# Kernel tuning notes

Hardware: AMD Instinct MI355X
Metric: run time of the kernel (lower is better)

## Reference

```python
import jax, jax.numpy as jnp
import numpy as np

C = 256
NH = 8
G = 32  # groupnorm groups (min(32, C))
EPS = 1e-6


def setup_inputs() -> dict:
    key = jax.random.key(0)
    ks = jax.random.split(key, 7)
    B, D, H, W = 2, 16, 16, 16
    x = jax.random.normal(ks[0], (B, C, D, H, W), dtype=jnp.float32)
    gn_gamma = jnp.ones((C,), jnp.float32)
    gn_beta = jnp.zeros((C,), jnp.float32)
    s = 1.0 / np.sqrt(C)
    qkv_w = jax.random.normal(ks[1], (3 * C, C), jnp.float32) * s  # 1x1x1 conv weight
    qkv_b = jnp.zeros((3 * C,), jnp.float32)
    proj_w = jax.random.normal(ks[2], (C, C), jnp.float32) * s
    proj_b = jnp.zeros((C,), jnp.float32)
    return {"x": x, "gn_gamma": gn_gamma, "gn_beta": gn_beta,
            "qkv_w": qkv_w, "qkv_b": qkv_b, "proj_w": proj_w, "proj_b": proj_b}


def _group_norm(x, gamma, beta):
    # x: [B, C, S]
    B, Cc, S = x.shape
    xg = x.reshape(B, G, (Cc // G) * S)
    mu = xg.mean(axis=-1, keepdims=True)
    var = xg.var(axis=-1, keepdims=True)
    xg = (xg - mu) * jax.lax.rsqrt(var + EPS)
    x = xg.reshape(B, Cc, S)
    return x * gamma[None, :, None] + beta[None, :, None]


def reference(x, gn_gamma, gn_beta, qkv_w, qkv_b, proj_w, proj_b):
    B, Cc, D, H, W = x.shape
    S = D * H * W
    hd = Cc // NH
    xf = x.reshape(B, Cc, S)
    h = _group_norm(xf, gn_gamma, gn_beta)
    # 1x1x1 conv == channel matmul: [B, 3C, S]
    qkv = jnp.einsum('oc,bcs->bos', qkv_w, h) + qkv_b[None, :, None]
    # torch path: reshape(B,3C,S).permute(0,2,1).chunk -> q=channels[0:C]
    q, k, v = qkv[:, :Cc], qkv[:, Cc:2 * Cc], qkv[:, 2 * Cc:]
    # [B, C, S] -> [B, NH, S, hd]
    def to_heads(t):
        return t.reshape(B, NH, hd, S).transpose(0, 1, 3, 2)
    q, k, v = to_heads(q), to_heads(k), to_heads(v)
    scale = hd ** (-0.5)
    attn = jax.nn.softmax(jnp.einsum('bnqd,bnkd->bnqk', q, k) * scale, axis=-1)
    o = jnp.einsum('bnqk,bnkd->bnqd', attn, v)  # [B, NH, S, hd]
    o = o.transpose(0, 1, 3, 2).reshape(B, Cc, S)  # back to [B, C, S]
    o = jnp.einsum('oc,bcs->bos', proj_w, o) + proj_b[None, :, None]
    return x + o.reshape(B, Cc, D, H, W)
```

## Files before the change

### kernel.cpp

```cpp
#include <hip/hip_runtime.h>
#include <cstddef>

#define S_LEN 4096
#define C_DIM 256
#define NHEADS 8
#define HDIM 32

typedef __attribute__((ext_vector_type(8))) _Float16 half8;
typedef __attribute__((ext_vector_type(4))) _Float16 half4;
typedef __attribute__((ext_vector_type(2))) _Float16 h2t;
typedef __attribute__((ext_vector_type(2))) __fp16 fp16x2;
typedef __attribute__((ext_vector_type(4))) float floatx4;

#define SC2F ((float)(0.17677669529663687 * 1.4426950408889634))

__global__ __launch_bounds__(256) void prep_stats(
    const float* __restrict__ qkv_w, const float* __restrict__ proj_w,
    const float* __restrict__ qkv_b, const float* __restrict__ x,
    _Float16* __restrict__ wq, _Float16* __restrict__ wp,
    float* __restrict__ qbias, float* __restrict__ gstat)
{
  const int blk = blockIdx.x;
  const int tid = threadIdx.x;
  if (blk < 64) {
    __shared__ float red[2][4];
    const int g = blk & 31, b = blk >> 5;
    const float* xb = x + ((size_t)b * C_DIM + g * 8) * S_LEN;
    const float4* x4 = (const float4*)xb;
    float sum = 0.f, sumsq = 0.f;
    for (int i = tid; i < 8192; i += 256) {
      float4 v = x4[i];
      sum += v.x + v.y + v.z + v.w;
      sumsq += v.x * v.x + v.y * v.y + v.z * v.z + v.w * v.w;
    }
    for (int off = 1; off < 64; off <<= 1) {
      sum += __shfl_xor(sum, off, 64);
      sumsq += __shfl_xor(sumsq, off, 64);
    }
    const int wv = tid >> 6, lane = tid & 63;
    if (lane == 0) { red[0][wv] = sum; red[1][wv] = sumsq; }
    __syncthreads();
    if (tid == 0) {
      float s = red[0][0] + red[0][1] + red[0][2] + red[0][3];
      float sq = red[1][0] + red[1][1] + red[1][2] + red[1][3];
      float mean = s * (1.f / 32768.f);
      float var = sq * (1.f / 32768.f) - mean * mean;
      gstat[((size_t)b * 32 + g) * 2 + 0] = mean;
      gstat[((size_t)b * 32 + g) * 2 + 1] = rsqrtf(var + 1e-6f);
    }
  } else {
    int idx = (blk - 64) * 256 + tid;
    if (idx < 768 * 256) {
      float v = qkv_w[idx];
      if (idx < 256 * 256) v *= SC2F;
      wq[idx] = (_Float16)v;
    } else if (idx < 768 * 256 + 256 * 256) {
      int i = idx - 768 * 256;
      wp[i] = (_Float16)proj_w[i];
    } else if (idx < 768 * 256 + 256 * 256 + 768) {
      int i = idx - (768 * 256 + 256 * 256);
      float bv = qkv_b[i];
      if (i < 256) bv *= SC2F;
      qbias[i] = bv;
    }
  }
}

__global__ __launch_bounds__(256) void qkv_gn_gemm(
    const _Float16* __restrict__ W, const float* __restrict__ bias,
    const float* __restrict__ x, const float* __restrict__ gamma,
    const float* __restrict__ beta, const float* __restrict__ gstat,
    _Float16* __restrict__ qo, _Float16* __restrict__ ko_,
    _Float16* __restrict__ vo)
{
  __shared__ __align__(16) _Float16 Ld[64 * 264];
  const int tid = threadIdx.x;
  const int b = blockIdx.z;
  const int s0 = blockIdx.y * 64;

  {
    const int c0 = (tid & 127) * 2, c1 = c0 + 1;
    const int sh = tid >> 7;
    const int g = c0 >> 3;
    const float mean = gstat[((size_t)b * 32 + g) * 2 + 0];
    const float rstd = gstat[((size_t)b * 32 + g) * 2 + 1];
    const float ga0 = gamma[c0] * rstd, be0 = beta[c0] - mean * ga0;
    const float ga1 = gamma[c1] * rstd, be1 = beta[c1] - mean * ga1;
    const float4* xa = (const float4*)(x + ((size_t)b * C_DIM + c0) * S_LEN + s0 + sh * 32);
    const float4* xc = (const float4*)(x + ((size_t)b * C_DIM + c1) * S_LEN + s0 + sh * 32);
    #pragma unroll
    for (int j = 0; j < 8; ++j) {
      float4 a = xa[j], c = xc[j];
      int sl = sh * 32 + j * 4;
      *(h2t*)&Ld[(sl + 0) * 264 + c0] = (h2t){ (_Float16)(a.x * ga0 + be0), (_Float16)(c.x * ga1 + be1) };
      *(h2t*)&Ld[(sl + 1) * 264 + c0] = (h2t){ (_Float16)(a.y * ga0 + be0), (_Float16)(c.y * ga1 + be1) };
      *(h2t*)&Ld[(sl + 2) * 264 + c0] = (h2t){ (_Float16)(a.z * ga0 + be0), (_Float16)(c.z * ga1 + be1) };
      *(h2t*)&Ld[(sl + 3) * 264 + c0] = (h2t){ (_Float16)(a.w * ga0 + be0), (_Float16)(c.w * ga1 + be1) };
    }
  }
  __syncthreads();

  const int lane = tid & 63, wv = tid >> 6;
  const int m = lane & 15, quad = lane >> 4;
  const int mt = blockIdx.x * 4 + wv;
  const int row = mt * 16 + m;
  const _Float16* wrow = W + (size_t)row * C_DIM + quad * 8;
  const _Float16* l0p = &Ld[m * 264 + quad * 8];
  const _Float16* l1p = l0p + 16 * 264;
  const _Float16* l2p = l0p + 32 * 264;
  const _Float16* l3p = l0p + 48 * 264;

  floatx4 acc0 = {0.f,0.f,0.f,0.f}, acc1 = acc0, acc2 = acc0, acc3 = acc0;
  half8 af = *(const half8*)wrow;
  #pragma unroll
  for (int k0 = 0; k0 < C_DIM; k0 += 32) {
    half8 afn;
    if (k0 < C_DIM - 32) afn = *(const half8*)(wrow + k0 + 32);
    half8 b0 = *(const half8*)(l0p + k0);
    half8 b1 = *(const half8*)(l1p + k0);
    half8 b2 = *(const half8*)(l2p + k0);
    half8 b3 = *(const half8*)(l3p + k0);
    acc0 = __builtin_amdgcn_mfma_f32_16x16x32_f16(af, b0, acc0, 0, 0, 0);
    acc1 = __builtin_amdgcn_mfma_f32_16x16x32_f16(af, b1, acc1, 0, 0, 0);
    acc2 = __builtin_amdgcn_mfma_f32_16x16x32_f16(af, b2, acc2, 0, 0, 0);
    acc3 = __builtin_amdgcn_mfma_f32_16x16x32_f16(af, b3, acc3, 0, 0, 0);
    af = afn;
  }
  floatx4 accs[4] = {acc0, acc1, acc2, acc3};
  const int ob = mt * 16 + quad * 4;
  const float bv0 = bias[ob], bv1 = bias[ob + 1],
              bv2 = bias[ob + 2], bv3 = bias[ob + 3];
  #pragma unroll
  for (int sub = 0; sub < 4; ++sub) {
    int s = s0 + sub * 16 + m;
    float v0 = accs[sub][0] + bv0, v1 = accs[sub][1] + bv1,
          v2 = accs[sub][2] + bv2, v3 = accs[sub][3] + bv3;
    if (ob < 512) {
      _Float16* dst = (ob < 256) ? qo : ko_;
      int oo = ob & 255, n = oo >> 5, d0 = oo & 31;
      half4 h = { (_Float16)v0, (_Float16)v1, (_Float16)v2, (_Float16)v3 };
      *(half4*)(dst + (((size_t)b * NHEADS + n) * S_LEN + s) * HDIM + d0) = h;
    } else {
      int oo = ob - 512, n = oo >> 5, d0 = oo & 31;
      _Float16* dst = vo + ((size_t)b * NHEADS + n) * HDIM * S_LEN + s;
      dst[(size_t)(d0 + 0) * S_LEN] = (_Float16)v0;
      dst[(size_t)(d0 + 1) * S_LEN] = (_Float16)v1;
      dst[(size_t)(d0 + 2) * S_LEN] = (_Float16)v2;
      dst[(size_t)(d0 + 3) * S_LEN] = (_Float16)v3;
    }
  }
}

__global__ __launch_bounds__(512) void attn_kernel(
    const _Float16* __restrict__ q, const _Float16* __restrict__ k,
    const _Float16* __restrict__ v, _Float16* __restrict__ o_t)
{
  __shared__ __align__(16) _Float16 Kl[2][64 * 40];
  __shared__ __align__(16) _Float16 Vl[2][32 * 68];
  const int tid = threadIdx.x;
  const int lane = tid & 63, wv = tid >> 6;
  const int m = lane & 15, quad = lane >> 4;
  const int n = blockIdx.y, b = blockIdx.z;
  const int q0 = blockIdx.x * 128 + wv * 16;

  const _Float16* qb = q + (size_t)(b * NHEADS + n) * S_LEN * HDIM;
  const _Float16* kb = k + (size_t)(b * NHEADS + n) * S_LEN * HDIM;
  const _Float16* vb = v + (size_t)(b * NHEADS + n) * HDIM * S_LEN;

  half8 qf = *(const half8*)(qb + (size_t)(q0 + m) * HDIM + quad * 8);

  const int krow = wv * 8 + (lane >> 3), kc = (lane & 7) * 4;
  const int vrow = wv * 4 + (lane >> 4), vc = (lane & 15) * 4;
  const _Float16* kg = kb + (size_t)krow * HDIM + kc;
  const _Float16* vg = vb + (size_t)vrow * S_LEN + vc;
  const int klds = krow * 40 + kc;
  const int vlds = vrow * 68 + vc;

  int2 kreg = *(const int2*)kg;
  int2 vreg = *(const int2*)vg;
  const _Float16* kgp = kg + 64 * HDIM;
  const _Float16* vgp = vg + 64;

  floatx4 o0 = {0.f,0.f,0.f,0.f}, o1 = o0;
  float l0 = 0.f;
  const fp16x2 one2 = { (__fp16)1.0f, (__fp16)1.0f };

  #pragma unroll 2
  for (int it = 0; it < 64; ++it) {
    const int bufi = it & 1;
    *(int2*)(&Kl[bufi][klds]) = kreg;
    *(int2*)(&Vl[bufi][vlds]) = vreg;
    kreg = *(const int2*)kgp; kgp += 64 * HDIM;
    vreg = *(const int2*)vgp; vgp += 64;
    __syncthreads();
    const _Float16* Kb = Kl[bufi];
    const _Float16* Vb = Vl[bufi];
    #pragma unroll
    for (int t = 0; t < 4; ++t) {
      half8 kf = *(const half8*)(Kb + (t * 16 + m) * 40 + quad * 8);
      half4 vf0 = *(const half4*)(Vb + m * 68 + t * 16 + quad * 4);
      half4 vf1 = *(const half4*)(Vb + (16 + m) * 68 + t * 16 + quad * 4);
      floatx4 z = {0.f,0.f,0.f,0.f};
      floatx4 s0 = __builtin_amdgcn_mfma_f32_16x16x32_f16(kf, qf, z, 0, 0, 0);
      float e0 = __builtin_amdgcn_exp2f(s0[0]);
      float e1 = __builtin_amdgcn_exp2f(s0[1]);
      float e2 = __builtin_amdgcn_exp2f(s0[2]);
      float e3 = __builtin_amdgcn_exp2f(s0[3]);
      half4 p0;
      fp16x2 plo = __builtin_amdgcn_cvt_pkrtz(e0, e1);
      fp16x2 phi = __builtin_amdgcn_cvt_pkrtz(e2, e3);
      *(fp16x2*)&p0 = plo;
      *((fp16x2*)&p0 + 1) = phi;
      l0 = __builtin_amdgcn_fdot2(plo, one2, l0, false);
      l0 = __builtin_amdgcn_fdot2(phi, one2, l0, false);
      o0 = __builtin_amdgcn_mfma_f32_16x16x16f16(vf0, p0, o0, 0, 0, 0);
      o1 = __builtin_amdgcn_mfma_f32_16x16x16f16(vf1, p0, o1, 0, 0, 0);
    }
  }
  l0 += __shfl_xor(l0, 16, 64);
  l0 += __shfl_xor(l0, 32, 64);
  const float i0 = 1.f / l0;
  const int c0 = n * HDIM + quad * 4;
  half4 h0 = { (_Float16)(o0[0]*i0), (_Float16)(o0[1]*i0),
               (_Float16)(o0[2]*i0), (_Float16)(o0[3]*i0) };
  half4 h1 = { (_Float16)(o1[0]*i0), (_Float16)(o1[1]*i0),
               (_Float16)(o1[2]*i0), (_Float16)(o1[3]*i0) };
  size_t base = ((size_t)b * S_LEN + q0 + m) * C_DIM + c0;
  *(half4*)(o_t + base) = h0;
  *(half4*)(o_t + base + 16) = h1;
}

__global__ __launch_bounds__(256) void proj_gemm(
    const _Float16* __restrict__ W, const float* __restrict__ bias,
    const _Float16* __restrict__ o_t, const float* __restrict__ x,
    float* __restrict__ out)
{
  const int tid = threadIdx.x;
  const int lane = tid & 63, wv = tid >> 6;
  const int m = lane & 15, quad = lane >> 4;
  const int mt = blockIdx.x * 4 + wv;
  const int s0 = blockIdx.y * 64;
  const int b = blockIdx.z;
  const int row = mt * 16 + m;
  const _Float16* ob = o_t + (size_t)b * S_LEN * C_DIM;

  const _Float16* wrow = W + (size_t)row * C_DIM + quad * 8;
  const _Float16* h0 = ob + (size_t)(s0 + m) * C_DIM + quad * 8;
  const _Float16* h1 = h0 + 16 * C_DIM;
  const _Float16* h2 = h0 + 32 * C_DIM;
  const _Float16* h3 = h0 + 48 * C_DIM;

  floatx4 acc0 = {0.f,0.f,0.f,0.f}, acc1 = acc0, acc2 = acc0, acc3 = acc0;
  half8 af = *(const half8*)wrow;
  half8 b0 = *(const half8*)h0;
  half8 b1 = *(const half8*)h1;
  half8 b2 = *(const half8*)h2;
  half8 b3 = *(const half8*)h3;
  #pragma unroll
  for (int k0 = 0; k0 < C_DIM; k0 += 32) {
    half8 afn, b0n, b1n, b2n, b3n;
    if (k0 < C_DIM - 32) {
      afn = *(const half8*)(wrow + k0 + 32);
      b0n = *(const half8*)(h0 + k0 + 32);
      b1n = *(const half8*)(h1 + k0 + 32);
      b2n = *(const half8*)(h2 + k0 + 32);
      b3n = *(const half8*)(h3 + k0 + 32);
    }
    acc0 = __builtin_amdgcn_mfma_f32_16x16x32_f16(af, b0, acc0, 0, 0, 0);
    acc1 = __builtin_amdgcn_mfma_f32_16x16x32_f16(af, b1, acc1, 0, 0, 0);
    acc2 = __builtin_amdgcn_mfma_f32_16x16x32_f16(af, b2, acc2, 0, 0, 0);
    acc3 = __builtin_amdgcn_mfma_f32_16x16x32_f16(af, b3, acc3, 0, 0, 0);
    af = afn; b0 = b0n; b1 = b1n; b2 = b2n; b3 = b3n;
  }
  floatx4 accs[4] = {acc0, acc1, acc2, acc3};
  #pragma unroll
  for (int sub = 0; sub < 4; ++sub) {
    int s = s0 + sub * 16 + m;
    #pragma unroll
    for (int r = 0; r < 4; ++r) {
      int c = mt * 16 + quad * 4 + r;
      size_t idx = ((size_t)b * C_DIM + c) * S_LEN + s;
      out[idx] = x[idx] + accs[sub][r] + bias[c];
    }
  }
}

extern "C" void kernel_launch(void* const* d_in, const int* in_sizes, int n_in,
                              void* d_out, int out_size, void* d_ws, size_t ws_size,
                              hipStream_t stream) {
  const float* x        = (const float*)d_in[0];
  const float* gn_gamma = (const float*)d_in[1];
  const float* gn_beta  = (const float*)d_in[2];
  const float* qkv_w    = (const float*)d_in[3];
  const float* qkv_b    = (const float*)d_in[4];
  const float* proj_w   = (const float*)d_in[5];
  const float* proj_b   = (const float*)d_in[6];
  float* out = (float*)d_out;

  const size_t n1 = (size_t)2 * S_LEN * C_DIM;
  char* ws = (char*)d_ws;
  _Float16* o_t = (_Float16*)ws;
  _Float16* qx  = o_t + n1;
  _Float16* kx  = qx + n1;
  _Float16* vx  = kx + n1;
  _Float16* wq  = vx + n1;
  _Float16* wp  = wq + 768 * 256;
  float*    qbias = (float*)(wp + 256 * 256);
  float*    gstat = qbias + 768;

  prep_stats<<<1091, 256, 0, stream>>>(qkv_w, proj_w, qkv_b, x, wq, wp, qbias, gstat);
  qkv_gn_gemm<<<dim3(12, 64, 2), 256, 0, stream>>>(wq, qbias, x, gn_gamma, gn_beta, gstat, qx, kx, vx);
  attn_kernel<<<dim3(32, 8, 2), 512, 0, stream>>>(qx, kx, vx, o_t);
  proj_gemm<<<dim3(4, 64, 2), 256, 0, stream>>>(wp, proj_b, o_t, x, out);
}
```

Before: 167.1 us.

## Enlarge per-warp tiles in QKV GEMM and attention to raise operand reuse

In the QKV GEMM, each warp now computes four 16-row output tiles against the same four LDS B fragments. The grid shrinks from 12 to 3 blocks in x, so the group-norm staging of x into LDS is done a quarter as often. In attention, each 256-thread block has 4 warps that each handle 32 queries (two Q fragments) over 128-key K/V tiles, with 16-byte loads and half as many barriers. This reuses K/V fragments across two query tiles and amortises staging. The cost is higher register pressure and fewer waves per block, and with only 384 GEMM blocks the lower block count may hurt latency hiding.

```diff
diff --git a/kernel.cpp b/kernel.cpp
--- a/kernel.cpp
+++ b/kernel.cpp
@@ -102,132 +102,181 @@
 
   const int lane = tid & 63, wv = tid >> 6;
   const int m = lane & 15, quad = lane >> 4;
-  const int mt = blockIdx.x * 4 + wv;
-  const int row = mt * 16 + m;
-  const _Float16* wrow = W + (size_t)row * C_DIM + quad * 8;
-  const _Float16* l0p = &Ld[m * 264 + quad * 8];
-  const _Float16* l1p = l0p + 16 * 264;
-  const _Float16* l2p = l0p + 32 * 264;
-  const _Float16* l3p = l0p + 48 * 264;
-
-  floatx4 acc0 = {0.f,0.f,0.f,0.f}, acc1 = acc0, acc2 = acc0, acc3 = acc0;
-  half8 af = *(const half8*)wrow;
+  const int mtb = blockIdx.x * 16 + wv * 4;
+  const _Float16* wrow0 = W + (size_t)((mtb + 0) * 16 + m) * C_DIM + quad * 8;
+  const _Float16* wrow1 = W + (size_t)((mtb + 1) * 16 + m) * C_DIM + quad * 8;
+  const _Float16* wrow2 = W + (size_t)((mtb + 2) * 16 + m) * C_DIM + quad * 8;
+  const _Float16* wrow3 = W + (size_t)((mtb + 3) * 16 + m) * C_DIM + quad * 8;
+  const _Float16* lp = &Ld[m * 264 + quad * 8];
+
+  floatx4 acc[4][4];
+  #pragma unroll
+  for (int j = 0; j < 4; ++j)
+    #pragma unroll
+    for (int s = 0; s < 4; ++s) acc[j][s] = (floatx4){0.f,0.f,0.f,0.f};
+
   #pragma unroll
   for (int k0 = 0; k0 < C_DIM; k0 += 32) {
-    half8 afn;
-    if (k0 < C_DIM - 32) afn = *(const half8*)(wrow + k0 + 32);
-    half8 b0 = *(const half8*)(l0p + k0);
-    half8 b1 = *(const half8*)(l1p + k0);
-    half8 b2 = *(const half8*)(l2p + k0);
-    half8 b3 = *(const half8*)(l3p + k0);
-    acc0 = __builtin_amdgcn_mfma_f32_16x16x32_f16(af, b0, acc0, 0, 0, 0);
-    acc1 = __builtin_amdgcn_mfma_f32_16x16x32_f16(af, b1, acc1, 0, 0, 0);
-    acc2 = __builtin_amdgcn_mfma_f32_16x16x32_f16(af, b2, acc2, 0, 0, 0);
-    acc3 = __builtin_amdgcn_mfma_f32_16x16x32_f16(af, b3, acc3, 0, 0, 0);
-    af = afn;
-  }
-  floatx4 accs[4] = {acc0, acc1, acc2, acc3};
-  const int ob = mt * 16 + quad * 4;
-  const float bv0 = bias[ob], bv1 = bias[ob + 1],
-              bv2 = bias[ob + 2], bv3 = bias[ob + 3];
-  #pragma unroll
-  for (int sub = 0; sub < 4; ++sub) {
-    int s = s0 + sub * 16 + m;
-    float v0 = accs[sub][0] + bv0, v1 = accs[sub][1] + bv1,
-          v2 = accs[sub][2] + bv2, v3 = accs[sub][3] + bv3;
-    if (ob < 512) {
-      _Float16* dst = (ob < 256) ? qo : ko_;
-      int oo = ob & 255, n = oo >> 5, d0 = oo & 31;
-      half4 h = { (_Float16)v0, (_Float16)v1, (_Float16)v2, (_Float16)v3 };
-      *(half4*)(dst + (((size_t)b * NHEADS + n) * S_LEN + s) * HDIM + d0) = h;
-    } else {
-      int oo = ob - 512, n = oo >> 5, d0 = oo & 31;
-      _Float16* dst = vo + ((size_t)b * NHEADS + n) * HDIM * S_LEN + s;
-      dst[(size_t)(d0 + 0) * S_LEN] = (_Float16)v0;
-      dst[(size_t)(d0 + 1) * S_LEN] = (_Float16)v1;
-      dst[(size_t)(d0 + 2) * S_LEN] = (_Float16)v2;
-      dst[(size_t)(d0 + 3) * S_LEN] = (_Float16)v3;
-    }
-  }
-}
-
-__global__ __launch_bounds__(512) void attn_kernel(
+    half8 b0 = *(const half8*)(lp + k0);
+    half8 b1 = *(const half8*)(lp + 16 * 264 + k0);
+    half8 b2 = *(const half8*)(lp + 32 * 264 + k0);
+    half8 b3 = *(const half8*)(lp + 48 * 264 + k0);
+    half8 a0 = *(const half8*)(wrow0 + k0);
+    half8 a1 = *(const half8*)(wrow1 + k0);
+    half8 a2 = *(const half8*)(wrow2 + k0);
+    half8 a3 = *(const half8*)(wrow3 + k0);
+    acc[0][0] = __builtin_amdgcn_mfma_f32_16x16x32_f16(a0, b0, acc[0][0], 0, 0, 0);
+    acc[0][1] = __builtin_amdgcn_mfma_f32_16x16x32_f16(a0, b1, acc[0][1], 0, 0, 0);
+    acc[0][2] = __builtin_amdgcn_mfma_f32_16x16x32_f16(a0, b2, acc[0][2], 0, 0, 0);
+    acc[0][3] = __builtin_amdgcn_mfma_f32_16x16x32_f16(a0, b3, acc[0][3], 0, 0, 0);
+    acc[1][0] = __builtin_amdgcn_mfma_f32_16x16x32_f16(a1, b0, acc[1][0], 0, 0, 0);
+    acc[1][1] = __builtin_amdgcn_mfma_f32_16x16x32_f16(a1, b1, acc[1][1], 0, 0, 0);
+    acc[1][2] = __builtin_amdgcn_mfma_f32_16x16x32_f16(a1, b2, acc[1][2], 0, 0, 0);
+    acc[1][3] = __builtin_amdgcn_mfma_f32_16x16x32_f16(a1, b3, acc[1][3], 0, 0, 0);
+    acc[2][0] = __builtin_amdgcn_mfma_f32_16x16x32_f16(a2, b0, acc[2][0], 0, 0, 0);
+    acc[2][1] = __builtin_amdgcn_mfma_f32_16x16x32_f16(a2, b1, acc[2][1], 0, 0, 0);
+    acc[2][2] = __builtin_amdgcn_mfma_f32_16x16x32_f16(a2, b2, acc[2][2], 0, 0, 0);
+    acc[2][3] = __builtin_amdgcn_mfma_f32_16x16x32_f16(a2, b3, acc[2][3], 0, 0, 0);
+    acc[3][0] = __builtin_amdgcn_mfma_f32_16x16x32_f16(a3, b0, acc[3][0], 0, 0, 0);
+    acc[3][1] = __builtin_amdgcn_mfma_f32_16x16x32_f16(a3, b1, acc[3][1], 0, 0, 0);
+    acc[3][2] = __builtin_amdgcn_mfma_f32_16x16x32_f16(a3, b2, acc[3][2], 0, 0, 0);
+    acc[3][3] = __builtin_amdgcn_mfma_f32_16x16x32_f16(a3, b3, acc[3][3], 0, 0, 0);
+  }
+
+  #pragma unroll
+  for (int j = 0; j < 4; ++j) {
+    const int ob = (mtb + j) * 16 + quad * 4;
+    const float bv0 = bias[ob], bv1 = bias[ob + 1],
+                bv2 = bias[ob + 2], bv3 = bias[ob + 3];
+    #pragma unroll
+    for (int sub = 0; sub < 4; ++sub) {
+      int s = s0 + sub * 16 + m;
+      float v0 = acc[j][sub][0] + bv0, v1 = acc[j][sub][1] + bv1,
+            v2 = acc[j][sub][2] + bv2, v3 = acc[j][sub][3] + bv3;
+      if (ob < 512) {
+        _Float16* dst = (ob < 256) ? qo : ko_;
+        int oo = ob & 255, n = oo >> 5, d0 = oo & 31;
+        half4 h = { (_Float16)v0, (_Float16)v1, (_Float16)v2, (_Float16)v3 };
+        *(half4*)(dst + (((size_t)b * NHEADS + n) * S_LEN + s) * HDIM + d0) = h;
+      } else {
+        int oo = ob - 512, n = oo >> 5, d0 = oo & 31;
+        _Float16* dst = vo + ((size_t)b * NHEADS + n) * HDIM * S_LEN + s;
+        dst[(size_t)(d0 + 0) * S_LEN] = (_Float16)v0;
+        dst[(size_t)(d0 + 1) * S_LEN] = (_Float16)v1;
+        dst[(size_t)(d0 + 2) * S_LEN] = (_Float16)v2;
+        dst[(size_t)(d0 + 3) * S_LEN] = (_Float16)v3;
+      }
+    }
+  }
+}
+
+__global__ __launch_bounds__(256) void attn_kernel(
     const _Float16* __restrict__ q, const _Float16* __restrict__ k,
     const _Float16* __restrict__ v, _Float16* __restrict__ o_t)
 {
-  __shared__ __align__(16) _Float16 Kl[2][64 * 40];
-  __shared__ __align__(16) _Float16 Vl[2][32 * 68];
+  __shared__ __align__(16) _Float16 Kl[2][128 * 40];
+  __shared__ __align__(16) _Float16 Vl[2][32 * 136];
   const int tid = threadIdx.x;
   const int lane = tid & 63, wv = tid >> 6;
   const int m = lane & 15, quad = lane >> 4;
   const int n = blockIdx.y, b = blockIdx.z;
-  const int q0 = blockIdx.x * 128 + wv * 16;
+  const int q0 = blockIdx.x * 128 + wv * 32;
 
   const _Float16* qb = q + (size_t)(b * NHEADS + n) * S_LEN * HDIM;
   const _Float16* kb = k + (size_t)(b * NHEADS + n) * S_LEN * HDIM;
   const _Float16* vb = v + (size_t)(b * NHEADS + n) * HDIM * S_LEN;
 
-  half8 qf = *(const half8*)(qb + (size_t)(q0 + m) * HDIM + quad * 8);
-
-  const int krow = wv * 8 + (lane >> 3), kc = (lane & 7) * 4;
-  const int vrow = wv * 4 + (lane >> 4), vc = (lane & 15) * 4;
-  const _Float16* kg = kb + (size_t)krow * HDIM + kc;
-  const _Float16* vg = vb + (size_t)vrow * S_LEN + vc;
-  const int klds = krow * 40 + kc;
-  const int vlds = vrow * 68 + vc;
-
-  int2 kreg = *(const int2*)kg;
-  int2 vreg = *(const int2*)vg;
-  const _Float16* kgp = kg + 64 * HDIM;
-  const _Float16* vgp = vg + 64;
-
-  floatx4 o0 = {0.f,0.f,0.f,0.f}, o1 = o0;
-  float l0 = 0.f;
+  half8 qf0 = *(const half8*)(qb + (size_t)(q0 + m) * HDIM + quad * 8);
+  half8 qf1 = *(const half8*)(qb + (size_t)(q0 + 16 + m) * HDIM + quad * 8);
+
+  const int krow = wv * 32 + (lane >> 1), kcol = (lane & 1) * 16;
+  const _Float16* kg = kb + (size_t)krow * HDIM + kcol;
+  const int klds = krow * 40 + kcol;
+  const int vrow = tid >> 3, vcol = (tid & 7) * 16;
+  const _Float16* vg = vb + (size_t)vrow * S_LEN + vcol;
+  const int vlds = vrow * 136 + vcol;
+
+  int4 kr0 = *(const int4*)kg;
+  int4 kr1 = *(const int4*)(kg + 8);
+  int4 vr0 = *(const int4*)vg;
+  int4 vr1 = *(const int4*)(vg + 8);
+  const _Float16* kgp = kg + 128 * HDIM;
+  const _Float16* vgp = vg + 128;
+
+  floatx4 o00 = {0.f,0.f,0.f,0.f}, o10 = o00, o01 = o00, o11 = o00;
+  float l0 = 0.f, l1 = 0.f;
   const fp16x2 one2 = { (__fp16)1.0f, (__fp16)1.0f };
 
   #pragma unroll 2
-  for (int it = 0; it < 64; ++it) {
+  for (int it = 0; it < 32; ++it) {
     const int bufi = it & 1;
-    *(int2*)(&Kl[bufi][klds]) = kreg;
-    *(int2*)(&Vl[bufi][vlds]) = vreg;
-    kreg = *(const int2*)kgp; kgp += 64 * HDIM;
-    vreg = *(const int2*)vgp; vgp += 64;
+    *(int4*)(&Kl[bufi][klds]) = kr0;
+    *(int4*)(&Kl[bufi][klds + 8]) = kr1;
+    *(int4*)(&Vl[bufi][vlds]) = vr0;
+    *(int4*)(&Vl[bufi][vlds + 8]) = vr1;
+    kr0 = *(const int4*)kgp;
+    kr1 = *(const int4*)(kgp + 8);
+    vr0 = *(const int4*)vgp;
+    vr1 = *(const int4*)(vgp + 8);
+    kgp += 128 * HDIM; vgp += 128;
     __syncthreads();
     const _Float16* Kb = Kl[bufi];
     const _Float16* Vb = Vl[bufi];
     #pragma unroll
-    for (int t = 0; t < 4; ++t) {
+    for (int t = 0; t < 8; ++t) {
       half8 kf = *(const half8*)(Kb + (t * 16 + m) * 40 + quad * 8);
-      half4 vf0 = *(const half4*)(Vb + m * 68 + t * 16 + quad * 4);
-      half4 vf1 = *(const half4*)(Vb + (16 + m) * 68 + t * 16 + quad * 4);
+      half4 vf0 = *(const half4*)(Vb + m * 136 + t * 16 + quad * 4);
+      half4 vf1 = *(const half4*)(Vb + (16 + m) * 136 + t * 16 + quad * 4);
       floatx4 z = {0.f,0.f,0.f,0.f};
-      floatx4 s0 = __builtin_amdgcn_mfma_f32_16x16x32_f16(kf, qf, z, 0, 0, 0);
-      float e0 = __builtin_amdgcn_exp2f(s0[0]);
-      float e1 = __builtin_amdgcn_exp2f(s0[1]);
-      float e2 = __builtin_amdgcn_exp2f(s0[2]);
-      float e3 = __builtin_amdgcn_exp2f(s0[3]);
-      half4 p0;
-      fp16x2 plo = __builtin_amdgcn_cvt_pkrtz(e0, e1);
-      fp16x2 phi = __builtin_amdgcn_cvt_pkrtz(e2, e3);
-      *(fp16x2*)&p0 = plo;
-      *((fp16x2*)&p0 + 1) = phi;
-      l0 = __builtin_amdgcn_fdot2(plo, one2, l0, false);
-      l0 = __builtin_amdgcn_fdot2(phi, one2, l0, false);
-      o0 = __builtin_amdgcn_mfma_f32_16x16x16f16(vf0, p0, o0, 0, 0, 0);
-      o1 = __builtin_amdgcn_mfma_f32_16x16x16f16(vf1, p0, o1, 0, 0, 0);
-    }
-  }
-  l0 += __shfl_xor(l0, 16, 64);
-  l0 += __shfl_xor(l0, 32, 64);
-  const float i0 = 1.f / l0;
+      floatx4 s0 = __builtin_amdgcn_mfma_f32_16x16x32_f16(kf, qf0, z, 0, 0, 0);
+      floatx4 s1 = __builtin_amdgcn_mfma_f32_16x16x32_f16(kf, qf1, z, 0, 0, 0);
+      float e00 = __builtin_amdgcn_exp2f(s0[0]);
+      float e01 = __builtin_amdgcn_exp2f(s0[1]);
+      float e02 = __builtin_amdgcn_exp2f(s0[2]);
+      float e03 = __builtin_amdgcn_exp2f(s0[3]);
+      float e10 = __builtin_amdgcn_exp2f(s1[0]);
+      float e11 = __builtin_amdgcn_exp2f(s1[1]);
+      float e12 = __builtin_amdgcn_exp2f(s1[2]);
+      float e13 = __builtin_amdgcn_exp2f(s1[3]);
+      half4 p0, p1;
+      fp16x2 p0lo = __builtin_amdgcn_cvt_pkrtz(e00, e01);
+      fp16x2 p0hi = __builtin_amdgcn_cvt_pkrtz(e02, e03);
+      fp16x2 p1lo = __builtin_amdgcn_cvt_pkrtz(e10, e11);
+      fp16x2 p1hi = __builtin_amdgcn_cvt_pkrtz(e12, e13);
+      *(fp16x2*)&p0 = p0lo; *((fp16x2*)&p0 + 1) = p0hi;
+      *(fp16x2*)&p1 = p1lo; *((fp16x2*)&p1 + 1) = p1hi;
+      l0 = __builtin_amdgcn_fdot2(p0lo, one2, l0, false);
+      l0 = __builtin_amdgcn_fdot2(p0hi, one2, l0, false);
+      l1 = __builtin_amdgcn_fdot2(p1lo, one2, l1, false);
+      l1 = __builtin_amdgcn_fdot2(p1hi, one2, l1, false);
+      o00 = __builtin_amdgcn_mfma_f32_16x16x16f16(vf0, p0, o00, 0, 0, 0);
+      o10 = __builtin_amdgcn_mfma_f32_16x16x16f16(vf1, p0, o10, 0, 0, 0);
+      o01 = __builtin_amdgcn_mfma_f32_16x16x16f16(vf0, p1, o01, 0, 0, 0);
+      o11 = __builtin_amdgcn_mfma_f32_16x16x16f16(vf1, p1, o11, 0, 0, 0);
+    }
+  }
+  l0 += __shfl_xor(l0, 16, 64); l0 += __shfl_xor(l0, 32, 64);
+  l1 += __shfl_xor(l1, 16, 64); l1 += __shfl_xor(l1, 32, 64);
+  const float i0 = 1.f / l0, i1 = 1.f / l1;
   const int c0 = n * HDIM + quad * 4;
-  half4 h0 = { (_Float16)(o0[0]*i0), (_Float16)(o0[1]*i0),
-               (_Float16)(o0[2]*i0), (_Float16)(o0[3]*i0) };
-  half4 h1 = { (_Float16)(o1[0]*i0), (_Float16)(o1[1]*i0),
-               (_Float16)(o1[2]*i0), (_Float16)(o1[3]*i0) };
-  size_t base = ((size_t)b * S_LEN + q0 + m) * C_DIM + c0;
-  *(half4*)(o_t + base) = h0;
-  *(half4*)(o_t + base + 16) = h1;
+  {
+    half4 h0 = { (_Float16)(o00[0]*i0), (_Float16)(o00[1]*i0),
+                 (_Float16)(o00[2]*i0), (_Float16)(o00[3]*i0) };
+    half4 h1 = { (_Float16)(o10[0]*i0), (_Float16)(o10[1]*i0),
+                 (_Float16)(o10[2]*i0), (_Float16)(o10[3]*i0) };
+    size_t base = ((size_t)b * S_LEN + q0 + m) * C_DIM + c0;
+    *(half4*)(o_t + base) = h0;
+    *(half4*)(o_t + base + 16) = h1;
+  }
+  {
+    half4 h0 = { (_Float16)(o01[0]*i1), (_Float16)(o01[1]*i1),
+                 (_Float16)(o01[2]*i1), (_Float16)(o01[3]*i1) };
+    half4 h1 = { (_Float16)(o11[0]*i1), (_Float16)(o11[1]*i1),
+                 (_Float16)(o11[2]*i1), (_Float16)(o11[3]*i1) };
+    size_t base = ((size_t)b * S_LEN + q0 + 16 + m) * C_DIM + c0;
+    *(half4*)(o_t + base) = h0;
+    *(half4*)(o_t + base + 16) = h1;
+  }
 }
 
 __global__ __launch_bounds__(256) void proj_gemm(
@@ -309,7 +358,7 @@
   float*    gstat = qbias + 768;
 
   prep_stats<<<1091, 256, 0, stream>>>(qkv_w, proj_w, qkv_b, x, wq, wp, qbias, gstat);
-  qkv_gn_gemm<<<dim3(12, 64, 2), 256, 0, stream>>>(wq, qbias, x, gn_gamma, gn_beta, gstat, qx, kx, vx);
-  attn_kernel<<<dim3(32, 8, 2), 512, 0, stream>>>(qx, kx, vx, o_t);
+  qkv_gn_gemm<<<dim3(3, 64, 2), 256, 0, stream>>>(wq, qbias, x, gn_gamma, gn_beta, gstat, qx, kx, vx);
+  attn_kernel<<<dim3(32, 8, 2), 256, 0, stream>>>(qx, kx, vx, o_t);
   proj_gemm<<<dim3(4, 64, 2), 256, 0, stream>>>(wp, proj_b, o_t, x, out);
 }
```

Result: no change. 167.6 us (+0.3%).

## Split attention over two KV halves with merge kernel; widen QKV GEMM tiles

Applied to the files above, without the earlier changes.

Attention now splits the key/value sequence into two halves across separate blocks, doubling the grid. Each block writes unnormalized partial outputs and row sums, and a new merge kernel combines them and normalizes. This relies on there being no running-max subtraction, so the halves add directly. The QKV GEMM also gives each wave two 16-row M tiles, halving its grid and reusing LDS B fragments, at the cost of an extra launch and extra partial-output traffic.

```diff
diff --git a/kernel.cpp b/kernel.cpp
--- a/kernel.cpp
+++ b/kernel.cpp
@@ -102,58 +102,66 @@
 
   const int lane = tid & 63, wv = tid >> 6;
   const int m = lane & 15, quad = lane >> 4;
-  const int mt = blockIdx.x * 4 + wv;
-  const int row = mt * 16 + m;
-  const _Float16* wrow = W + (size_t)row * C_DIM + quad * 8;
-  const _Float16* l0p = &Ld[m * 264 + quad * 8];
-  const _Float16* l1p = l0p + 16 * 264;
-  const _Float16* l2p = l0p + 32 * 264;
-  const _Float16* l3p = l0p + 48 * 264;
-
-  floatx4 acc0 = {0.f,0.f,0.f,0.f}, acc1 = acc0, acc2 = acc0, acc3 = acc0;
-  half8 af = *(const half8*)wrow;
+  const int mtb = blockIdx.x * 8 + wv * 2;
+  const _Float16* wrow0 = W + (size_t)((mtb + 0) * 16 + m) * C_DIM + quad * 8;
+  const _Float16* wrow1 = W + (size_t)((mtb + 1) * 16 + m) * C_DIM + quad * 8;
+  const _Float16* lp = &Ld[m * 264 + quad * 8];
+
+  floatx4 acc[2][4];
+  #pragma unroll
+  for (int j = 0; j < 2; ++j)
+    #pragma unroll
+    for (int s = 0; s < 4; ++s) acc[j][s] = (floatx4){0.f,0.f,0.f,0.f};
+
   #pragma unroll
   for (int k0 = 0; k0 < C_DIM; k0 += 32) {
-    half8 afn;
-    if (k0 < C_DIM - 32) afn = *(const half8*)(wrow + k0 + 32);
-    half8 b0 = *(const half8*)(l0p + k0);
-    half8 b1 = *(const half8*)(l1p + k0);
-    half8 b2 = *(const half8*)(l2p + k0);
-    half8 b3 = *(const half8*)(l3p + k0);
-    acc0 = __builtin_amdgcn_mfma_f32_16x16x32_f16(af, b0, acc0, 0, 0, 0);
-    acc1 = __builtin_amdgcn_mfma_f32_16x16x32_f16(af, b1, acc1, 0, 0, 0);
-    acc2 = __builtin_amdgcn_mfma_f32_16x16x32_f16(af, b2, acc2, 0, 0, 0);
-    acc3 = __builtin_amdgcn_mfma_f32_16x16x32_f16(af, b3, acc3, 0, 0, 0);
-    af = afn;
-  }
-  floatx4 accs[4] = {acc0, acc1, acc2, acc3};
-  const int ob = mt * 16 + quad * 4;
-  const float bv0 = bias[ob], bv1 = bias[ob + 1],
-              bv2 = bias[ob + 2], bv3 = bias[ob + 3];
-  #pragma unroll
-  for (int sub = 0; sub < 4; ++sub) {
-    int s = s0 + sub * 16 + m;
-    float v0 = accs[sub][0] + bv0, v1 = accs[sub][1] + bv1,
-          v2 = accs[sub][2] + bv2, v3 = accs[sub][3] + bv3;
-    if (ob < 512) {
-      _Float16* dst = (ob < 256) ? qo : ko_;
-      int oo = ob & 255, n = oo >> 5, d0 = oo & 31;
-      half4 h = { (_Float16)v0, (_Float16)v1, (_Float16)v2, (_Float16)v3 };
-      *(half4*)(dst + (((size_t)b * NHEADS + n) * S_LEN + s) * HDIM + d0) = h;
-    } else {
-      int oo = ob - 512, n = oo >> 5, d0 = oo & 31;
-      _Float16* dst = vo + ((size_t)b * NHEADS + n) * HDIM * S_LEN + s;
-      dst[(size_t)(d0 + 0) * S_LEN] = (_Float16)v0;
-      dst[(size_t)(d0 + 1) * S_LEN] = (_Float16)v1;
-      dst[(size_t)(d0 + 2) * S_LEN] = (_Float16)v2;
-      dst[(size_t)(d0 + 3) * S_LEN] = (_Float16)v3;
+    half8 b0 = *(const half8*)(lp + k0);
+    half8 b1 = *(const half8*)(lp + 16 * 264 + k0);
+    half8 b2 = *(const half8*)(lp + 32 * 264 + k0);
+    half8 b3 = *(const half8*)(lp + 48 * 264 + k0);
+    half8 a0 = *(const half8*)(wrow0 + k0);
+    half8 a1 = *(const half8*)(wrow1 + k0);
+    acc[0][0] = __builtin_amdgcn_mfma_f32_16x16x32_f16(a0, b0, acc[0][0], 0, 0, 0);
+    acc[0][1] = __builtin_amdgcn_mfma_f32_16x16x32_f16(a0, b1, acc[0][1], 0, 0, 0);
+    acc[0][2] = __builtin_amdgcn_mfma_f32_16x16x32_f16(a0, b2, acc[0][2], 0, 0, 0);
+    acc[0][3] = __builtin_amdgcn_mfma_f32_16x16x32_f16(a0, b3, acc[0][3], 0, 0, 0);
+    acc[1][0] = __builtin_amdgcn_mfma_f32_16x16x32_f16(a1, b0, acc[1][0], 0, 0, 0);
+    acc[1][1] = __builtin_amdgcn_mfma_f32_16x16x32_f16(a1, b1, acc[1][1], 0, 0, 0);
+    acc[1][2] = __builtin_amdgcn_mfma_f32_16x16x32_f16(a1, b2, acc[1][2], 0, 0, 0);
+    acc[1][3] = __builtin_amdgcn_mfma_f32_16x16x32_f16(a1, b3, acc[1][3], 0, 0, 0);
+  }
+
+  #pragma unroll
+  for (int j = 0; j < 2; ++j) {
+    const int ob = (mtb + j) * 16 + quad * 4;
+    const float bv0 = bias[ob], bv1 = bias[ob + 1],
+                bv2 = bias[ob + 2], bv3 = bias[ob + 3];
+    #pragma unroll
+    for (int sub = 0; sub < 4; ++sub) {
+      int s = s0 + sub * 16 + m;
+      float v0 = acc[j][sub][0] + bv0, v1 = acc[j][sub][1] + bv1,
+            v2 = acc[j][sub][2] + bv2, v3 = acc[j][sub][3] + bv3;
+      if (ob < 512) {
+        _Float16* dst = (ob < 256) ? qo : ko_;
+        int oo = ob & 255, n = oo >> 5, d0 = oo & 31;
+        half4 h = { (_Float16)v0, (_Float16)v1, (_Float16)v2, (_Float16)v3 };
+        *(half4*)(dst + (((size_t)b * NHEADS + n) * S_LEN + s) * HDIM + d0) = h;
+      } else {
+        int oo = ob - 512, n = oo >> 5, d0 = oo & 31;
+        _Float16* dst = vo + ((size_t)b * NHEADS + n) * HDIM * S_LEN + s;
+        dst[(size_t)(d0 + 0) * S_LEN] = (_Float16)v0;
+        dst[(size_t)(d0 + 1) * S_LEN] = (_Float16)v1;
+        dst[(size_t)(d0 + 2) * S_LEN] = (_Float16)v2;
+        dst[(size_t)(d0 + 3) * S_LEN] = (_Float16)v3;
+      }
     }
   }
 }
 
 __global__ __launch_bounds__(512) void attn_kernel(
     const _Float16* __restrict__ q, const _Float16* __restrict__ k,
-    const _Float16* __restrict__ v, _Float16* __restrict__ o_t)
+    const _Float16* __restrict__ v, _Float16* __restrict__ po,
+    float* __restrict__ pl)
 {
   __shared__ __align__(16) _Float16 Kl[2][64 * 40];
   __shared__ __align__(16) _Float16 Vl[2][32 * 68];
@@ -161,11 +169,13 @@
   const int lane = tid & 63, wv = tid >> 6;
   const int m = lane & 15, quad = lane >> 4;
   const int n = blockIdx.y, b = blockIdx.z;
-  const int q0 = blockIdx.x * 128 + wv * 16;
-
-  const _Float16* qb = q + (size_t)(b * NHEADS + n) * S_LEN * HDIM;
-  const _Float16* kb = k + (size_t)(b * NHEADS + n) * S_LEN * HDIM;
-  const _Float16* vb = v + (size_t)(b * NHEADS + n) * HDIM * S_LEN;
+  const int qc = blockIdx.x >> 1, kh = blockIdx.x & 1;
+  const int q0 = qc * 128 + wv * 16;
+  const int bh = b * NHEADS + n;
+
+  const _Float16* qb = q + (size_t)bh * S_LEN * HDIM;
+  const _Float16* kb = k + (size_t)bh * S_LEN * HDIM + (size_t)kh * 2048 * HDIM;
+  const _Float16* vb = v + (size_t)bh * HDIM * S_LEN + (size_t)kh * 2048;
 
   half8 qf = *(const half8*)(qb + (size_t)(q0 + m) * HDIM + quad * 8);
 
@@ -186,7 +196,7 @@
   const fp16x2 one2 = { (__fp16)1.0f, (__fp16)1.0f };
 
   #pragma unroll 2
-  for (int it = 0; it < 64; ++it) {
+  for (int it = 0; it < 32; ++it) {
     const int bufi = it & 1;
     *(int2*)(&Kl[bufi][klds]) = kreg;
     *(int2*)(&Vl[bufi][vlds]) = vreg;
@@ -219,15 +229,32 @@
   }
   l0 += __shfl_xor(l0, 16, 64);
   l0 += __shfl_xor(l0, 32, 64);
-  const float i0 = 1.f / l0;
-  const int c0 = n * HDIM + quad * 4;
-  half4 h0 = { (_Float16)(o0[0]*i0), (_Float16)(o0[1]*i0),
-               (_Float16)(o0[2]*i0), (_Float16)(o0[3]*i0) };
-  half4 h1 = { (_Float16)(o1[0]*i0), (_Float16)(o1[1]*i0),
-               (_Float16)(o1[2]*i0), (_Float16)(o1[3]*i0) };
-  size_t base = ((size_t)b * S_LEN + q0 + m) * C_DIM + c0;
-  *(half4*)(o_t + base) = h0;
-  *(half4*)(o_t + base + 16) = h1;
+  _Float16* poh = po + (size_t)kh * 2097152 + ((size_t)bh * S_LEN + q0 + m) * HDIM;
+  half4 h0 = { (_Float16)o0[0], (_Float16)o0[1], (_Float16)o0[2], (_Float16)o0[3] };
+  half4 h1 = { (_Float16)o1[0], (_Float16)o1[1], (_Float16)o1[2], (_Float16)o1[3] };
+  *(half4*)(poh + quad * 4) = h0;
+  *(half4*)(poh + 16 + quad * 4) = h1;
+  if (quad == 0) pl[(size_t)kh * 65536 + (size_t)bh * S_LEN + q0 + m] = l0;
+}
+
+__global__ __launch_bounds__(256) void attn_merge(
+    const _Float16* __restrict__ po, const float* __restrict__ pl,
+    _Float16* __restrict__ o_t)
+{
+  const int tid = threadIdx.x;
+  const int row = blockIdx.x * 64 + (tid >> 2);
+  const int d0 = (tid & 3) * 8;
+  const int bh = row >> 12, qq = row & 4095;
+  const int b = bh >> 3, n = bh & 7;
+  const float l = pl[row] + pl[65536 + row];
+  const float inv = 1.f / l;
+  half8 a = *(const half8*)(po + (size_t)row * HDIM + d0);
+  half8 c = *(const half8*)(po + 2097152 + (size_t)row * HDIM + d0);
+  half8 o;
+  #pragma unroll
+  for (int i = 0; i < 8; ++i)
+    o[i] = (_Float16)(((float)a[i] + (float)c[i]) * inv);
+  *(half8*)(o_t + ((size_t)b * S_LEN + qq) * C_DIM + n * HDIM + d0) = o;
 }
 
 __global__ __launch_bounds__(256) void proj_gemm(
@@ -307,9 +334,12 @@
   _Float16* wp  = wq + 768 * 256;
   float*    qbias = (float*)(wp + 256 * 256);
   float*    gstat = qbias + 768;
+  _Float16* po  = (_Float16*)(gstat + 128);
+  float*    pl  = (float*)(po + 2 * n1);
 
   prep_stats<<<1091, 256, 0, stream>>>(qkv_w, proj_w, qkv_b, x, wq, wp, qbias, gstat);
-  qkv_gn_gemm<<<dim3(12, 64, 2), 256, 0, stream>>>(wq, qbias, x, gn_gamma, gn_beta, gstat, qx, kx, vx);
-  attn_kernel<<<dim3(32, 8, 2), 512, 0, stream>>>(qx, kx, vx, o_t);
+  qkv_gn_gemm<<<dim3(6, 64, 2), 256, 0, stream>>>(wq, qbias, x, gn_gamma, gn_beta, gstat, qx, kx, vx);
+  attn_kernel<<<dim3(64, 8, 2), 512, 0, stream>>>(qx, kx, vx, po, pl);
+  attn_merge<<<1024, 256, 0, stream>>>(po, pl, o_t);
   proj_gemm<<<dim3(4, 64, 2), 256, 0, stream>>>(wp, proj_b, o_t, x, out);
 }
```

Result: no change. 166.1 us (-0.6%).
